# Optimization experiments

Measured on AMD Instinct MI355X. Metric: run time of the kernel, lower is better.

Reference implementation:

```python
import jax, jax.numpy as jnp
import numpy as np

BN_EPS = 1e-5


def _batchnorm(x, gamma, beta):
    # training-mode BatchNorm2d: biased batch stats over (N, H, W)
    mean = jnp.mean(x, axis=(0, 2, 3), keepdims=True)
    var = jnp.var(x, axis=(0, 2, 3), keepdims=True)
    xn = (x - mean) * jax.lax.rsqrt(var + BN_EPS)
    return xn * gamma[None, :, None, None] + beta[None, :, None, None]


def _bin_weight(w):
    # BitConv2d_Robust: w_bin = sign(w) * mean(|w|) per output channel (STE in fwd is just the value)
    alpha = jnp.mean(jnp.abs(w), axis=(1, 2, 3), keepdims=True)
    return jax.lax.stop_gradient(jnp.sign(w) * alpha - w) + w


def _conv(x, w, b, pad):
    y = jax.lax.conv_general_dilated(
        x, w, window_strides=(1, 1), padding=[(pad, pad), (pad, pad)],
        dimension_numbers=('NCHW', 'OIHW', 'NCHW'))
    return y + b[None, :, None, None]


def setup_inputs() -> dict:
    key = jax.random.key(0)
    ks = jax.random.split(key, 14)
    B, Cin, Cout, T, H, W = 16, 128, 256, 512, 64, 64
    fan1 = Cin * 9
    fan2 = Cout * 9
    return {
        'x': jax.random.normal(ks[0], (B, Cin, H, W), jnp.float32),
        't': jax.random.normal(ks[1], (B, T), jnp.float32),
        'bn1_g': jnp.ones((Cin,), jnp.float32),
        'bn1_b': jnp.zeros((Cin,), jnp.float32),
        'w1': jax.random.normal(ks[2], (Cout, Cin, 3, 3), jnp.float32) / np.sqrt(fan1),
        'b1': jax.random.normal(ks[3], (Cout,), jnp.float32) * 0.01,
        'tW': jax.random.normal(ks[4], (Cout, T), jnp.float32) / np.sqrt(T),
        'tb': jax.random.normal(ks[5], (Cout,), jnp.float32) * 0.01,
        'bn2_g': jnp.ones((Cout,), jnp.float32),
        'bn2_b': jnp.zeros((Cout,), jnp.float32),
        'w2': jax.random.normal(ks[6], (Cout, Cout, 3, 3), jnp.float32) / np.sqrt(fan2),
        'b2': jax.random.normal(ks[7], (Cout,), jnp.float32) * 0.01,
        'ws': jax.random.normal(ks[8], (Cout, Cin, 1, 1), jnp.float32) / np.sqrt(Cin),
        'bs': jax.random.normal(ks[9], (Cout,), jnp.float32) * 0.01,
    }


def reference(x, t, bn1_g, bn1_b, w1, b1, tW, tb, bn2_g, bn2_b, w2, b2, ws, bs):
    h = jnp.sign(_batchnorm(x, bn1_g, bn1_b))                # BN + sign binarize
    h = _conv(h, _bin_weight(w1), b1, pad=1)                  # binarized 3x3 conv
    temb = t @ tW.T + tb                                      # time MLP -> [B, Cout]
    h = h + temb[:, :, None, None]
    h = jnp.sign(_batchnorm(h, bn2_g, bn2_b))
    h = _conv(h, _bin_weight(w2), b2, pad=1)
    skip = _conv(x, _bin_weight(ws), bs, pad=0)               # 1x1 binarized skip (in_ch != out_ch)
    return h + skip
```

## Files before the change

kernel.cpp:

```cpp
#include <hip/hip_runtime.h>
#include <stdint.h>

typedef unsigned int uint;
typedef short bf16x8 __attribute__((ext_vector_type(8)));
typedef float f32x4 __attribute__((ext_vector_type(4)));

#define EPS 1e-5f


__global__ __launch_bounds__(256) void k_bn1_part(const float* __restrict__ x, float* __restrict__ part) {
  int c = blockIdx.x, chunk = blockIdx.y;
  float s = 0.f, s2 = 0.f;
  #pragma unroll
  for (int jb = 0; jb < 2; ++jb) {
    int b = chunk * 2 + jb;
    const float4* xb = (const float4*)(x + (((size_t)((b << 7) | c)) << 12));
    #pragma unroll
    for (int k = 0; k < 4; ++k) {
      float4 q = xb[k * 256 + threadIdx.x];
      s += (q.x + q.y) + (q.z + q.w);
      s2 += q.x * q.x + q.y * q.y + q.z * q.z + q.w * q.w;
    }
  }
  #pragma unroll
  for (int off = 32; off > 0; off >>= 1) { s += __shfl_down(s, off); s2 += __shfl_down(s2, off); }
  __shared__ float ls[4], ls2[4];
  int wid = threadIdx.x >> 6, lane = threadIdx.x & 63;
  if (lane == 0) { ls[wid] = s; ls2[wid] = s2; }
  __syncthreads();
  if (threadIdx.x == 0) {
    part[(c * 8 + chunk) * 2 + 0] = ls[0] + ls[1] + ls[2] + ls[3];
    part[(c * 8 + chunk) * 2 + 1] = ls2[0] + ls2[1] + ls2[2] + ls2[3];
  }
}

__global__ void k_bn1_fin(const float* __restrict__ part, const float* __restrict__ g,
                          const float* __restrict__ be, float* __restrict__ sc, float* __restrict__ sh) {
  int c = threadIdx.x;
  float s = 0.f, s2 = 0.f;
  for (int k = 0; k < 8; ++k) { s += part[(c * 8 + k) * 2]; s2 += part[(c * 8 + k) * 2 + 1]; }
  const float inv = 1.f / 65536.f;
  float m = s * inv, var = s2 * inv - m * m;
  float rs = rsqrtf(var + EPS);
  float scale = rs * g[c];
  sc[c] = scale;
  sh[c] = be[c] - m * scale;
}

__global__ __launch_bounds__(128) void k_packw1(const float* __restrict__ w1, uint* __restrict__ wb,
                                                float* __restrict__ alpha, ushort* __restrict__ wT1) {
  int co = blockIdx.x, wid = threadIdx.x >> 6, lane = threadIdx.x & 63;
  int ci = threadIdx.x;
  const float* wp = w1 + (co * 128 + ci) * 9;
  float wv[9]; float s = 0.f;
  #pragma unroll
  for (int tp = 0; tp < 9; ++tp) { wv[tp] = wp[tp]; s += fabsf(wv[tp]); }
  #pragma unroll
  for (int tp = 0; tp < 9; ++tp) {
    wT1[(((tp << 2) + (ci >> 5)) << 13) + (co << 5) + (ci & 31)] = (wv[tp] > 0.f) ? 0x3F80u : 0xBF80u;
    unsigned long long m = __ballot(wv[tp] > 0.f);
    if (lane == 0) {
      wb[(co * 9 + tp) * 4 + wid * 2 + 0] = (uint)m;
      wb[(co * 9 + tp) * 4 + wid * 2 + 1] = (uint)(m >> 32);
    }
  }
  #pragma unroll
  for (int off = 32; off > 0; off >>= 1) s += __shfl_down(s, off);
  __shared__ float l2[2];
  if (lane == 0) l2[wid] = s;
  __syncthreads();
  if (threadIdx.x == 0) alpha[co] = (l2[0] + l2[1]) * (1.f / 1152.f);
}

__global__ __launch_bounds__(256) void k_packw2(const float* __restrict__ w2, uint* __restrict__ wb,
                                                float* __restrict__ alpha, ushort* __restrict__ wT) {
  int co = blockIdx.x, wid = threadIdx.x >> 6, lane = threadIdx.x & 63;
  int ci = threadIdx.x;
  const float* wp = w2 + (co * 256 + ci) * 9;
  float wv[9]; float s = 0.f;
  #pragma unroll
  for (int tp = 0; tp < 9; ++tp) { wv[tp] = wp[tp]; s += fabsf(wv[tp]); }
  int chunk = ci >> 7, kc = (ci >> 5) & 3, cil = ci & 31;
  #pragma unroll
  for (int tp = 0; tp < 9; ++tp) {
    wT[(((tp << 3) + (chunk << 2) + kc) << 13) + (co << 5) + cil] = (wv[tp] > 0.f) ? 0x3F80u : 0xBF80u;
    unsigned long long m = __ballot(wv[tp] > 0.f);
    if (lane == 0) {
      wb[(co * 9 + tp) * 8 + wid * 2 + 0] = (uint)m;
      wb[(co * 9 + tp) * 8 + wid * 2 + 1] = (uint)(m >> 32);
    }
  }
  #pragma unroll
  for (int off = 32; off > 0; off >>= 1) s += __shfl_down(s, off);
  __shared__ float l4[4];
  if (lane == 0) l4[wid] = s;
  __syncthreads();
  if (threadIdx.x == 0) alpha[co] = (l4[0] + l4[1] + l4[2] + l4[3]) * (1.f / 2304.f);
}

__global__ __launch_bounds__(256) void k_base(const uint* __restrict__ wb1, const uint* __restrict__ wb2,
                                              int* __restrict__ base1, int* __restrict__ base2) {
  int co = threadIdx.x;
  int pc1[9], pc2[9];
  #pragma unroll
  for (int tp = 0; tp < 9; ++tp) {
    uint a = 0;
    #pragma unroll
    for (int k = 0; k < 4; ++k) a += __popc(wb1[co * 36 + tp * 4 + k]);
    pc1[tp] = (int)a;
    uint b = 0;
    #pragma unroll
    for (int k = 0; k < 8; ++k) b += __popc(wb2[co * 72 + tp * 8 + k]);
    pc2[tp] = (int)b;
  }
  #pragma unroll
  for (int pat = 0; pat < 9; ++pat) {
    int yt = pat / 3, xt = pat % 3;
    int b1v = 1152, b2v = 2304;
    #pragma unroll
    for (int tp = 0; tp < 9; ++tp) {
      int dy = tp / 3 - 1, dx = tp % 3 - 1;
      bool inv = (dy < 0 && yt == 0) || (dy > 0 && yt == 2) || (dx < 0 && xt == 0) || (dx > 0 && xt == 2);
      if (inv) { b1v -= 128 - 2 * pc1[tp]; b2v -= 256 - 2 * pc2[tp]; }
    }
    base1[pat * 256 + co] = b1v;
    base2[pat * 256 + co] = b2v;
  }
}

__global__ __launch_bounds__(128) void k_packws(const float* __restrict__ wsk, float* __restrict__ swT) {
  int co = blockIdx.x, ci = threadIdx.x;
  float v = wsk[co * 128 + ci];
  float s = fabsf(v);
  #pragma unroll
  for (int off = 32; off > 0; off >>= 1) s += __shfl_down(s, off);
  __shared__ float l2[2]; __shared__ float tot;
  int wid = threadIdx.x >> 6, lane = threadIdx.x & 63;
  if (lane == 0) l2[wid] = s;
  __syncthreads();
  if (threadIdx.x == 0) tot = (l2[0] + l2[1]) * (1.f / 128.f);
  __syncthreads();
  float a = tot;
  swT[ci * 256 + co] = (v > 0.f) ? a : -a;
}

__global__ __launch_bounds__(256) void k_temb(const float* __restrict__ t, const float* __restrict__ tW,
                                              const float* __restrict__ tbias, float* __restrict__ temb) {
  int b = blockIdx.x, co = threadIdx.x;
  const float* tr = t + b * 512;
  const float* wr = tW + co * 512;
  float a0 = 0, a1 = 0, a2 = 0, a3 = 0;
  #pragma unroll 8
  for (int k = 0; k < 512; k += 4) {
    a0 = fmaf(tr[k + 0], wr[k + 0], a0);
    a1 = fmaf(tr[k + 1], wr[k + 1], a1);
    a2 = fmaf(tr[k + 2], wr[k + 2], a2);
    a3 = fmaf(tr[k + 3], wr[k + 3], a3);
  }
  temb[b * 256 + co] = (a0 + a1) + (a2 + a3) + tbias[co];
}

__global__ __launch_bounds__(256, 2) void k_skip(const float* __restrict__ x, const float* __restrict__ swT,
                                                 const float* __restrict__ bsk, const float* __restrict__ b2,
                                                 const float* __restrict__ sc1, const float* __restrict__ sh1,
                                                 uint* __restrict__ sbinw, ushort* __restrict__ h1w,
                                                 int mfma1, float* __restrict__ out) {
  __shared__ float xs[32 * 136];
  __shared__ float wsl[32 * 128];
  int s = blockIdx.x;
  int b = s >> 5;
  int px0 = (s & 31) << 7;
  int co0 = blockIdx.y << 7;
  int t = threadIdx.x;
  int tx = t & 15, ty = t >> 4;

  float4 acc[8][2];
  #pragma unroll
  for (int i = 0; i < 8; ++i) { acc[i][0] = make_float4(0, 0, 0, 0); acc[i][1] = make_float4(0, 0, 0, 0); }

  #pragma unroll 1
  for (int kc = 0; kc < 4; ++kc) {
    if (kc) __syncthreads();
    #pragma unroll
    for (int k2 = 0; k2 < 4; ++k2) {
      int idx = k2 * 256 + t;
      int ci_l = idx >> 5, pxl = (idx & 31) << 2;
      float4 v = *(const float4*)(x + (((size_t)((b << 7) | (kc * 32 + ci_l))) << 12) + px0 + pxl);
      int g = pxl >> 3;
      *(float4*)&xs[ci_l * 136 + g * 8 + ((g >> 2) << 1) + (pxl & 7)] = v;
    }
    #pragma unroll
    for (int k2 = 0; k2 < 4; ++k2) {
      int idx = k2 * 256 + t;
      int ci_l = idx >> 5, col = (idx & 31) << 2;
      *(float4*)&wsl[ci_l * 128 + col] = *(const float4*)(swT + (size_t)(kc * 32 + ci_l) * 256 + co0 + col);
    }
    __syncthreads();

    if (blockIdx.y == 0 && t < 128) {
      int pxl = t;
      int g = pxl >> 3;
      int xo = g * 8 + ((g >> 2) << 1) + (pxl & 7);
      if (mfma1) {
        ushort hv[32];
        #pragma unroll
        for (int i = 0; i < 32; ++i) {
          int ci = kc * 32 + i;
          float v = xs[i * 136 + xo];
          hv[i] = ((v * sc1[ci] + sh1[ci]) > 0.f) ? (ushort)0x3F80u : (ushort)0xBF80u;
        }
        uint4* dst = (uint4*)(h1w + (((size_t)((b << 12) | (px0 + pxl))) << 7) + (kc << 5));
        const uint4* srcv = (const uint4*)hv;
        dst[0] = srcv[0]; dst[1] = srcv[1]; dst[2] = srcv[2]; dst[3] = srcv[3];
      } else {
        uint accb = 0;
        #pragma unroll
        for (int i = 0; i < 32; ++i) {
          int ci = kc * 32 + i;
          float v = xs[i * 136 + xo];
          accb |= ((v * sc1[ci] + sh1[ci]) > 0.f ? 1u : 0u) << i;
        }
        sbinw[(((size_t)b << 12) | (px0 + pxl)) * 4 + kc] = accb;
      }
    }

    int xbase = tx * 8 + ((tx >> 2) << 1);
    int wbase = ty * 8;
    #pragma unroll 2
    for (int ci = 0; ci < 32; ++ci) {
      float4 xv0 = *(float4*)&xs[ci * 136 + xbase];
      float4 xv1 = *(float4*)&xs[ci * 136 + xbase + 4];
      float4 wv0 = *(float4*)&wsl[ci * 128 + wbase];
      float4 wv1 = *(float4*)&wsl[ci * 128 + wbase + 4];
      float wq[8] = {wv0.x, wv0.y, wv0.z, wv0.w, wv1.x, wv1.y, wv1.z, wv1.w};
      #pragma unroll
      for (int i = 0; i < 8; ++i) {
        acc[i][0].x = fmaf(wq[i], xv0.x, acc[i][0].x);
        acc[i][0].y = fmaf(wq[i], xv0.y, acc[i][0].y);
        acc[i][0].z = fmaf(wq[i], xv0.z, acc[i][0].z);
        acc[i][0].w = fmaf(wq[i], xv0.w, acc[i][0].w);
        acc[i][1].x = fmaf(wq[i], xv1.x, acc[i][1].x);
        acc[i][1].y = fmaf(wq[i], xv1.y, acc[i][1].y);
        acc[i][1].z = fmaf(wq[i], xv1.z, acc[i][1].z);
        acc[i][1].w = fmaf(wq[i], xv1.w, acc[i][1].w);
      }
    }
  }

  float* ob = out + ((size_t)b << 20) + px0 + tx * 8;
  #pragma unroll
  for (int i = 0; i < 8; ++i) {
    int co = co0 + ty * 8 + i;
    float bb = bsk[co] + b2[co];
    float4 r0 = acc[i][0]; r0.x += bb; r0.y += bb; r0.z += bb; r0.w += bb;
    float4 r1 = acc[i][1]; r1.x += bb; r1.y += bb; r1.z += bb; r1.w += bb;
    *(float4*)(ob + ((size_t)co << 12)) = r0;
    *(float4*)(ob + ((size_t)co << 12) + 4) = r1;
  }
}

__global__ __launch_bounds__(256, 2) void k_conv1_mfma(const ushort* __restrict__ h1,
                                                       const ushort* __restrict__ wT1,
                                                       short* __restrict__ S1,
                                                       float* __restrict__ part_s,
                                                       float* __restrict__ part_s2) {
  __shared__ ushort act[4 * 66 * 128];
  int bidx = blockIdx.x;
  int s = (bidx & 7) * 64 + (bidx >> 3);
  int b = s >> 5, y0 = (s & 31) << 1;
  int lane = threadIdx.x & 63, wave = threadIdx.x >> 6;
  int co0 = wave << 6;
  int l15 = lane & 15, lk = lane >> 4;

  f32x4 acc[4][8] = {};
  const uint4* h1g = (const uint4*)h1;
  uint4* a4 = (uint4*)act;
  const size_t abase = (size_t)((co0 + l15) << 5) + (lk << 3);

#define LOADAV(dst, ptr)                                                     \
  {                                                                          \
    _Pragma("unroll")                                                        \
    for (int ct_ = 0; ct_ < 4; ++ct_)                                        \
      dst[ct_] = *(const bf16x8*)((ptr) + abase + (ct_ << 9));               \
  }
#define KC_BLOCK(AV, kcv)                                                    \
  {                                                                          \
    _Pragma("unroll")                                                        \
    for (int r_ = 0; r_ < 2; ++r_) {                                         \
      bf16x8 Bv[4];                                                          \
      _Pragma("unroll")                                                      \
      for (int pt_ = 0; pt_ < 4; ++pt_) {                                    \
        int xi_ = (r_ + ty) * 66 + tx + pt_ * 16 + l15;                      \
        int u_ = (((xi_ << 4) + ((kcv) << 2) + lk) ^ (xi_ & 7));             \
        Bv[pt_] = *(bf16x8*)&act[u_ << 3];                                   \
      }                                                                      \
      _Pragma("unroll")                                                      \
      for (int ct_ = 0; ct_ < 4; ++ct_)                                      \
        _Pragma("unroll")                                                    \
        for (int pt_ = 0; pt_ < 4; ++pt_)                                    \
          acc[ct_][r_ * 4 + pt_] = __builtin_amdgcn_mfma_f32_16x16x32_bf16(  \
              AV[ct_], Bv[pt_], acc[ct_][r_ * 4 + pt_], 0, 0, 0);            \
    }                                                                        \
  }

  #pragma unroll 1
  for (int i = 0; i < 17; ++i) {
    int idx = i * 256 + threadIdx.x;
    if (idx < 4224) {
      int q = idx & 15, rowxz = idx >> 4;
      int xz = rowxz % 66, r = rowxz / 66;
      int yy = y0 + r - 1, xx = xz - 1;
      uint4 v = make_uint4(0, 0, 0, 0);
      if (((unsigned)yy < 64u) && ((unsigned)xx < 64u))
        v = h1g[(size_t)((b << 12) | (yy << 6) | xx) * 16 + q];
      a4[((rowxz << 4) + q) ^ (rowxz & 7)] = v;
    }
  }
  __syncthreads();

  bf16x8 AvA[4], AvB[4];
  LOADAV(AvA, wT1);
  #pragma unroll 1
  for (int tp = 0; tp < 9; ++tp) {
    int ty = tp / 3, tx = tp % 3;
    const ushort* wtp = wT1 + ((size_t)tp << 15);
    const ushort* wnx = (tp < 8) ? (wtp + (1 << 15)) : wtp;

    LOADAV(AvB, wtp + (1 << 13));  KC_BLOCK(AvA, 0);
    LOADAV(AvA, wtp + (2 << 13));  KC_BLOCK(AvB, 1);
    LOADAV(AvB, wtp + (3 << 13));  KC_BLOCK(AvA, 2);
    LOADAV(AvA, wnx);              KC_BLOCK(AvB, 3);
  }
#undef LOADAV
#undef KC_BLOCK

  #pragma unroll
  for (int ct = 0; ct < 4; ++ct)
    #pragma unroll
    for (int r = 0; r < 2; ++r)
      #pragma unroll
      for (int pt = 0; pt < 4; ++pt) {
        int x = pt * 16 + l15;
        short* ob = S1 + ((size_t)b << 20) + ((y0 + r) << 6) + x;
        #pragma unroll
        for (int j = 0; j < 4; ++j) {
          int co = co0 + ct * 16 + lk * 4 + j;
          ob[(size_t)co << 12] = (short)acc[ct][r * 4 + pt][j];
        }
      }
  #pragma unroll
  for (int ct = 0; ct < 4; ++ct) {
    float s1v[4] = {0, 0, 0, 0}, s2v[4] = {0, 0, 0, 0};
    #pragma unroll
    for (int k = 0; k < 8; ++k)
      #pragma unroll
      for (int j = 0; j < 4; ++j) {
        float v = acc[ct][k][j];
        s1v[j] += v; s2v[j] += v * v;
      }
    #pragma unroll
    for (int off = 1; off < 16; off <<= 1)
      #pragma unroll
      for (int j = 0; j < 4; ++j) {
        s1v[j] += __shfl_xor(s1v[j], off);
        s2v[j] += __shfl_xor(s2v[j], off);
      }
    if (l15 == 0) {
      #pragma unroll
      for (int j = 0; j < 4; ++j) {
        int co = co0 + ct * 16 + lk * 4 + j;
        part_s[(size_t)s * 256 + co] = s1v[j];
        part_s2[(size_t)s * 256 + co] = s2v[j];
      }
    }
  }
}

__global__ void k_bn2_fin2(const float* __restrict__ part_s, const float* __restrict__ part_s2,
                           const float* __restrict__ al1, const float* __restrict__ b1,
                           const float* __restrict__ g2, const float* __restrict__ be2,
                           const float* __restrict__ temb,
                           float* __restrict__ A, float* __restrict__ Bc, float* __restrict__ Cc) {
  int co = blockIdx.x;
  int t = threadIdx.x;
  float sS = 0.f, scS = 0.f, s2 = 0.f;
  for (int k = 0; k < 8; ++k) {
    int blk = t + k * 64;
    int b = blk >> 5;
    float c = b1[co] + temb[(b << 8) + co];
    float Sv = part_s[(size_t)blk * 256 + co];
    sS += Sv; scS += c * Sv; s2 += part_s2[(size_t)blk * 256 + co];
  }
  #pragma unroll
  for (int off = 32; off > 0; off >>= 1) {
    sS += __shfl_down(sS, off); scS += __shfl_down(scS, off); s2 += __shfl_down(s2, off);
  }
  if (t == 0) {
    float a = al1[co];
    float sumc = 0.f, sumc2 = 0.f;
    for (int b = 0; b < 16; ++b) { float c = b1[co] + temb[(b << 8) + co]; sumc += c; sumc2 += c * c; }
    float sumY = a * sS + 4096.f * sumc;
    float sumY2 = a * a * s2 + 2.f * a * scS + 4096.f * sumc2;
    const float inv = 1.f / 65536.f;
    float m = sumY * inv, var = sumY2 * inv - m * m;
    float rs = rsqrtf(var + EPS);
    float gg = rs * g2[co];
    A[co] = a * gg;
    Bc[co] = (b1[co] - m) * gg + be2[co];
    Cc[co] = gg;
  }
}

__global__ __launch_bounds__(256, 1) void k_conv1(const uint4* __restrict__ sbin, const uint* __restrict__ wb1,
                                                  const int* __restrict__ base1, short* __restrict__ S1) {
  __shared__ uint wlds[32 * 36];
  __shared__ int blds[9 * 32];
  int co0 = blockIdx.y << 5;
  #pragma unroll
  for (int k = 0; k < 4; ++k) wlds[k * 256 + threadIdx.x] = wb1[co0 * 36 + k * 256 + threadIdx.x];
  if (threadIdx.x < 128) wlds[1024 + threadIdx.x] = wb1[co0 * 36 + 1024 + threadIdx.x];
  #pragma unroll
  for (int k = 0; k < 2; ++k) {
    int idx = k * 256 + threadIdx.x;
    if (idx < 288) blds[idx] = base1[(idx >> 5) * 256 + co0 + (idx & 31)];
  }
  int bt = blockIdx.x;
  int b = bt >> 4;
  int y = ((bt & 15) << 2) | (threadIdx.x >> 6);
  int cx = threadIdx.x & 63;
  uint nb[9][4];
  #pragma unroll
  for (int dy = -1; dy <= 1; ++dy)
    #pragma unroll
    for (int dx = -1; dx <= 1; ++dx) {
      int tp = (dy + 1) * 3 + (dx + 1);
      int yy = y + dy, xx = cx + dx;
      bool v = ((unsigned)yy < 64u) && ((unsigned)xx < 64u);
      uint4 q = make_uint4(0, 0, 0, 0);
      if (v) q = sbin[(b << 12) | (yy << 6) | xx];
      nb[tp][0] = q.x; nb[tp][1] = q.y; nb[tp][2] = q.z; nb[tp][3] = q.w;
    }
  int pat = ((y == 0) ? 0 : ((y == 63) ? 6 : 3)) + ((cx == 0) ? 0 : ((cx == 63) ? 2 : 1));
  __syncthreads();
  int p = (y << 6) | cx;
  short* op = S1 + ((size_t)b << 20) + ((size_t)co0 << 12) + p;
  #pragma unroll 1
  for (int cc = 0; cc < 4; ++cc) {
    short accv[8];
    #pragma unroll
    for (int j = 0; j < 8; ++j) {
      int co_l = cc * 8 + j;
      const uint4* wp4 = (const uint4*)(wlds + co_l * 36);
      uint m0 = 0, m1 = 0, m2 = 0, m3 = 0;
      #pragma unroll
      for (int tp = 0; tp < 9; ++tp) {
        uint4 w4 = wp4[tp];
        m0 += __popc(nb[tp][0] ^ w4.x);
        m1 += __popc(nb[tp][1] ^ w4.y);
        m2 += __popc(nb[tp][2] ^ w4.z);
        m3 += __popc(nb[tp][3] ^ w4.w);
      }
      accv[j] = (short)(blds[pat * 32 + co_l] - 2 * (int)((m0 + m1) + (m2 + m3)));
    }
    #pragma unroll
    for (int j = 0; j < 8; ++j) op[(size_t)(cc * 8 + j) << 12] = accv[j];
  }
}

__global__ __launch_bounds__(256) void k_bn2_part(const short* __restrict__ S1, const float* __restrict__ al1,
                                                  const float* __restrict__ b1, const float* __restrict__ temb,
                                                  float* __restrict__ part) {
  int co = blockIdx.x, chunk = blockIdx.y;
  float a = al1[co], bb = b1[co];
  float s = 0.f, s2 = 0.f;
  #pragma unroll
  for (int jb = 0; jb < 2; ++jb) {
    int b = chunk * 2 + jb;
    float tb_ = bb + temb[(b << 8) | co];
    const uint4* sp = (const uint4*)(S1 + ((size_t)b << 20) + ((size_t)co << 12));
    #pragma unroll
    for (int k = 0; k < 2; ++k) {
      uint4 q = sp[k * 256 + threadIdx.x];
      uint ws[4] = {q.x, q.y, q.z, q.w};
      #pragma unroll
      for (int w = 0; w < 4; ++w) {
        float f0 = fmaf(a, (float)((short)(ws[w] & 0xffffu)), tb_);
        float f1 = fmaf(a, (float)((short)(ws[w] >> 16)), tb_);
        s += f0 + f1;
        s2 += f0 * f0 + f1 * f1;
      }
    }
  }
  #pragma unroll
  for (int off = 32; off > 0; off >>= 1) { s += __shfl_down(s, off); s2 += __shfl_down(s2, off); }
  __shared__ float ls[4], ls2[4];
  int wid = threadIdx.x >> 6, lane = threadIdx.x & 63;
  if (lane == 0) { ls[wid] = s; ls2[wid] = s2; }
  __syncthreads();
  if (threadIdx.x == 0) {
    part[(co * 8 + chunk) * 2 + 0] = ls[0] + ls[1] + ls[2] + ls[3];
    part[(co * 8 + chunk) * 2 + 1] = ls2[0] + ls2[1] + ls2[2] + ls2[3];
  }
}

__global__ void k_bn2_fin(const float* __restrict__ part, const float* __restrict__ al1,
                          const float* __restrict__ b1, const float* __restrict__ g2,
                          const float* __restrict__ be2, float* __restrict__ A,
                          float* __restrict__ Bc, float* __restrict__ Cc) {
  int co = threadIdx.x;
  float s = 0.f, s2 = 0.f;
  for (int k = 0; k < 8; ++k) { s += part[(co * 8 + k) * 2]; s2 += part[(co * 8 + k) * 2 + 1]; }
  const float inv = 1.f / 65536.f;
  float m = s * inv, var = s2 * inv - m * m;
  float rs = rsqrtf(var + EPS);
  float gg = rs * g2[co];
  A[co] = al1[co] * gg;
  Bc[co] = (b1[co] - m) * gg + be2[co];
  Cc[co] = gg;
}

__global__ __launch_bounds__(256) void k_bin2_bf16(const short* __restrict__ S1, const float* __restrict__ A,
                                                   const float* __restrict__ Bc, const float* __restrict__ Cc,
                                                   const float* __restrict__ temb, uint4* __restrict__ h2u4) {
  __shared__ uint4 tile[64 * 32];
  int b = blockIdx.x >> 6;
  int px0 = (blockIdx.x & 63) << 6;
  int pxl = threadIdx.x & 63, quad = threadIdx.x >> 6;
  const short* sp = S1 + ((size_t)b << 20) + (px0 + pxl);
  const float* tp = temb + (b << 8);
  #pragma unroll 1
  for (int g = 0; g < 8; ++g) {
    uint d[4];
    #pragma unroll
    for (int h = 0; h < 4; ++h) {
      int c0 = quad * 64 + g * 8 + h * 2;
      float v0 = A[c0] * (float)sp[(size_t)c0 << 12] + Bc[c0] + Cc[c0] * tp[c0];
      float v1 = A[c0 + 1] * (float)sp[(size_t)(c0 + 1) << 12] + Bc[c0 + 1] + Cc[c0 + 1] * tp[c0 + 1];
      uint s0 = (v0 > 0.f) ? 0x3F80u : 0xBF80u;
      uint s1 = (v1 > 0.f) ? 0x3F80u : 0xBF80u;
      d[h] = s0 | (s1 << 16);
    }
    int slot = quad * 8 + g;
    tile[pxl * 32 + (slot ^ (pxl & 7))] = make_uint4(d[0], d[1], d[2], d[3]);
  }
  __syncthreads();
  uint4* dst = h2u4 + ((size_t)(b << 12) + px0) * 32;
  #pragma unroll
  for (int k = 0; k < 8; ++k) {
    int c = k * 256 + threadIdx.x;
    int px = c >> 5, slot = c & 31;
    dst[c] = tile[px * 32 + (slot ^ (px & 7))];
  }
}

__global__ __launch_bounds__(256, 2) void k_conv2_mfma(const ushort* __restrict__ h2,
                                                       const ushort* __restrict__ wT,
                                                       const float* __restrict__ al2,
                                                       float* __restrict__ out) {
  __shared__ ushort act[4 * 66 * 128];
  int bidx = blockIdx.x;
  int s = (bidx & 7) * 64 + (bidx >> 3);
  int b = s >> 5, y0 = (s & 31) << 1;
  int lane = threadIdx.x & 63, wave = threadIdx.x >> 6;
  int co0 = wave << 6;
  int l15 = lane & 15, lk = lane >> 4;

  f32x4 acc[4][8] = {};
  const uint4* h2g = (const uint4*)h2;
  uint4* a4 = (uint4*)act;
  const size_t abase = (size_t)((co0 + l15) << 5) + (lk << 3);

#define LOADAV(dst, ptr)                                                     \
  {                                                                          \
    _Pragma("unroll")                                                        \
    for (int ct_ = 0; ct_ < 4; ++ct_)                                        \
      dst[ct_] = *(const bf16x8*)((ptr) + abase + (ct_ << 9));               \
  }
#define KC_BLOCK(AV, kcv)                                                    \
  {                                                                          \
    _Pragma("unroll")                                                        \
    for (int r_ = 0; r_ < 2; ++r_) {                                         \
      bf16x8 Bv[4];                                                          \
      _Pragma("unroll")                                                      \
      for (int pt_ = 0; pt_ < 4; ++pt_) {                                    \
        int xi_ = (r_ + ty) * 66 + tx + pt_ * 16 + l15;                      \
        int u_ = (((xi_ << 4) + ((kcv) << 2) + lk) ^ (xi_ & 7));             \
        Bv[pt_] = *(bf16x8*)&act[u_ << 3];                                   \
      }                                                                      \
      _Pragma("unroll")                                                      \
      for (int ct_ = 0; ct_ < 4; ++ct_)                                      \
        _Pragma("unroll")                                                    \
        for (int pt_ = 0; pt_ < 4; ++pt_)                                    \
          acc[ct_][r_ * 4 + pt_] = __builtin_amdgcn_mfma_f32_16x16x32_bf16(  \
              AV[ct_], Bv[pt_], acc[ct_][r_ * 4 + pt_], 0, 0, 0);            \
    }                                                                        \
  }

  #pragma unroll 1
  for (int chunk = 0; chunk < 2; ++chunk) {
    if (chunk) __syncthreads();
    #pragma unroll 1
    for (int i = 0; i < 17; ++i) {
      int idx = i * 256 + threadIdx.x;
      if (idx < 4224) {
        int q = idx & 15, rowxz = idx >> 4;
        int xz = rowxz % 66, r = rowxz / 66;
        int yy = y0 + r - 1, xx = xz - 1;
        uint4 v = make_uint4(0, 0, 0, 0);
        if (((unsigned)yy < 64u) && ((unsigned)xx < 64u))
          v = h2g[(size_t)((b << 12) | (yy << 6) | xx) * 32 + chunk * 16 + q];
        a4[((rowxz << 4) + q) ^ (rowxz & 7)] = v;
      }
    }
    __syncthreads();

    const ushort* wch = wT + ((size_t)chunk << 15);
    bf16x8 AvA[4], AvB[4];
    LOADAV(AvA, wch);

    #pragma unroll 1
    for (int tp = 0; tp < 9; ++tp) {
      int ty = tp / 3, tx = tp % 3;
      const ushort* wtp = wch + ((size_t)tp << 16);
      const ushort* wnx = (tp < 8) ? (wtp + (1 << 16)) : wtp;

      LOADAV(AvB, wtp + (1 << 13));  KC_BLOCK(AvA, 0);
      LOADAV(AvA, wtp + (2 << 13));  KC_BLOCK(AvB, 1);
      LOADAV(AvB, wtp + (3 << 13));  KC_BLOCK(AvA, 2);
      LOADAV(AvA, wnx);              KC_BLOCK(AvB, 3);
    }
  }
#undef LOADAV
#undef KC_BLOCK

  #pragma unroll
  for (int ct = 0; ct < 4; ++ct) {
    #pragma unroll
    for (int r = 0; r < 2; ++r) {
      #pragma unroll
      for (int pt = 0; pt < 4; ++pt) {
        int x = pt * 16 + l15;
        float* ob = out + ((size_t)b << 20) + ((y0 + r) << 6) + x;
        #pragma unroll
        for (int j = 0; j < 4; ++j) {
          int co = co0 + ct * 16 + lk * 4 + j;
          float* p = ob + ((size_t)co << 12);
          *p = fmaf(al2[co], acc[ct][r * 4 + pt][j], *p);
        }
      }
    }
  }
}

__global__ __launch_bounds__(256) void k_bin2_packed(const short* __restrict__ S1, const float* __restrict__ A,
                                                     const float* __restrict__ Bc, const float* __restrict__ Cc,
                                                     const float* __restrict__ temb, uint4* __restrict__ hbin) {
  int pg = blockIdx.x * 256 + threadIdx.x;
  int b = pg >> 12, p = pg & 4095;
  int c0 = blockIdx.y << 7;
  const short* sp = S1 + ((size_t)b << 20) + p;
  const float* tp = temb + (b << 8);
  uint w[4];
  #pragma unroll
  for (int wd = 0; wd < 4; ++wd) {
    uint acc = 0;
    #pragma unroll
    for (int i = 0; i < 32; ++i) {
      int co = c0 + wd * 32 + i;
      float v = A[co] * (float)sp[(size_t)co << 12] + Bc[co] + Cc[co] * tp[co];
      acc |= (v > 0.f ? 1u : 0u) << i;
    }
    w[wd] = acc;
  }
  hbin[pg * 2 + blockIdx.y] = make_uint4(w[0], w[1], w[2], w[3]);
}

__global__ __launch_bounds__(256, 1) void k_conv2_pop(const uint4* __restrict__ hbin, const uint* __restrict__ wb2,
                                                      const int* __restrict__ base2, const float* __restrict__ al2,
                                                      float* __restrict__ out) {
  __shared__ uint wlds[32 * 72];
  __shared__ int blds[9 * 32];
  int co0 = blockIdx.y << 5;
  #pragma unroll
  for (int k = 0; k < 9; ++k) wlds[k * 256 + threadIdx.x] = wb2[co0 * 72 + k * 256 + threadIdx.x];
  #pragma unroll
  for (int k = 0; k < 2; ++k) {
    int idx = k * 256 + threadIdx.x;
    if (idx < 288) blds[idx] = base2[(idx >> 5) * 256 + co0 + (idx & 31)];
  }
  int bt = blockIdx.x;
  int b = bt >> 4;
  int y = ((bt & 15) << 2) | (threadIdx.x >> 6);
  int cx = threadIdx.x & 63;
  uint nb[9][8];
  #pragma unroll
  for (int dy = -1; dy <= 1; ++dy)
    #pragma unroll
    for (int dx = -1; dx <= 1; ++dx) {
      int tp = (dy + 1) * 3 + (dx + 1);
      int yy = y + dy, xx = cx + dx;
      bool v = ((unsigned)yy < 64u) && ((unsigned)xx < 64u);
      uint4 q0 = make_uint4(0, 0, 0, 0), q1 = make_uint4(0, 0, 0, 0);
      if (v) {
        int pix = (b << 12) | (yy << 6) | xx;
        q0 = hbin[pix * 2 + 0];
        q1 = hbin[pix * 2 + 1];
      }
      nb[tp][0] = q0.x; nb[tp][1] = q0.y; nb[tp][2] = q0.z; nb[tp][3] = q0.w;
      nb[tp][4] = q1.x; nb[tp][5] = q1.y; nb[tp][6] = q1.z; nb[tp][7] = q1.w;
    }
  int pat = ((y == 0) ? 0 : ((y == 63) ? 6 : 3)) + ((cx == 0) ? 0 : ((cx == 63) ? 2 : 1));
  __syncthreads();
  int p = (y << 6) | cx;
  float* op = out + ((size_t)b << 20) + ((size_t)co0 << 12) + p;
  #pragma unroll 1
  for (int cc = 0; cc < 4; ++cc) {
    float ov[8];
    #pragma unroll
    for (int j = 0; j < 8; ++j) ov[j] = op[(size_t)(cc * 8 + j) << 12];
    #pragma unroll
    for (int j = 0; j < 8; ++j) {
      int co_l = cc * 8 + j;
      const uint4* wp4 = (const uint4*)(wlds + co_l * 72);
      uint m0 = 0, m1 = 0, m2 = 0, m3 = 0;
      #pragma unroll
      for (int tp = 0; tp < 9; ++tp) {
        uint4 wa = wp4[tp * 2 + 0];
        uint4 wb_ = wp4[tp * 2 + 1];
        m0 += __popc(nb[tp][0] ^ wa.x);
        m1 += __popc(nb[tp][1] ^ wa.y);
        m2 += __popc(nb[tp][2] ^ wa.z);
        m3 += __popc(nb[tp][3] ^ wa.w);
        m0 += __popc(nb[tp][4] ^ wb_.x);
        m1 += __popc(nb[tp][5] ^ wb_.y);
        m2 += __popc(nb[tp][6] ^ wb_.z);
        m3 += __popc(nb[tp][7] ^ wb_.w);
      }
      int acc = blds[pat * 32 + co_l] - 2 * (int)((m0 + m1) + (m2 + m3));
      ov[j] = fmaf(al2[co0 + co_l], (float)acc, ov[j]);
    }
    #pragma unroll
    for (int j = 0; j < 8; ++j) op[(size_t)(cc * 8 + j) << 12] = ov[j];
  }
}

extern "C" void kernel_launch(void* const* d_in, const int* in_sizes, int n_in,
                              void* d_out, int out_size, void* d_ws, size_t ws_size,
                              hipStream_t stream) {
  const float* x    = (const float*)d_in[0];
  const float* t    = (const float*)d_in[1];
  const float* bn1g = (const float*)d_in[2];
  const float* bn1b = (const float*)d_in[3];
  const float* w1   = (const float*)d_in[4];
  const float* b1   = (const float*)d_in[5];
  const float* tW   = (const float*)d_in[6];
  const float* tb   = (const float*)d_in[7];
  const float* bn2g = (const float*)d_in[8];
  const float* bn2b = (const float*)d_in[9];
  const float* w2   = (const float*)d_in[10];
  const float* b2   = (const float*)d_in[11];
  const float* wsk  = (const float*)d_in[12];
  const float* bsk  = (const float*)d_in[13];
  float* out = (float*)d_out;
  char* ws = (char*)d_ws;

  float* bn1part = (float*)(ws + 0);
  float* sc1     = (float*)(ws + 8192);
  float* sh1     = (float*)(ws + 8704);
  uint4* sbin    = (uint4*)(ws + 9216);
  uint*  wb1     = (uint*) (ws + 1057792);
  float* al1     = (float*)(ws + 1094656);
  uint*  wb2     = (uint*) (ws + 1095680);
  float* al2     = (float*)(ws + 1169408);
  float* swkT    = (float*)(ws + 1170432);
  float* temb    = (float*)(ws + 1301504);
  float* bn2part = (float*)(ws + 1317888);
  float* A2      = (float*)(ws + 1334272);
  float* Bc2     = (float*)(ws + 1335296);
  float* Cc2     = (float*)(ws + 1336320);
  int*   base1g  = (int*)  (ws + 1337344);
  int*   base2g  = (int*)  (ws + 1346560);
  uint4*  hbin    = (uint4*)(ws + 1355776);
  float*  part_s  = (float*)(ws + 1355776);
  float*  part_s2 = (float*)(ws + 1880064);
  ushort* wT1     = (ushort*)(ws + 2404352);
  ushort* wT2     = (ushort*)(ws + 3452928);
  short*  S1      = (short*)(ws + 4632576);
  ushort* h2      = (ushort*)(ws + 38187008);
  ushort* h1      = (ushort*)(ws + 71741440);
  const size_t WS_NEED2 = 71741440ULL;
  const size_t WS_NEED1 = 88518656ULL;
  bool mode2 = (ws_size >= WS_NEED2);
  bool mode1 = (ws_size >= WS_NEED1);

  k_bn1_part<<<dim3(128, 8), 256, 0, stream>>>(x, bn1part);
  k_bn1_fin<<<1, 128, 0, stream>>>(bn1part, bn1g, bn1b, sc1, sh1);
  k_packw1<<<256, 128, 0, stream>>>(w1, wb1, al1, wT1);
  k_packw2<<<256, 256, 0, stream>>>(w2, wb2, al2, wT2);
  k_base<<<1, 256, 0, stream>>>(wb1, wb2, base1g, base2g);
  k_packws<<<256, 128, 0, stream>>>(wsk, swkT);
  k_temb<<<16, 256, 0, stream>>>(t, tW, tb, temb);
  k_skip<<<dim3(512, 2), 256, 0, stream>>>(x, swkT, bsk, b2, sc1, sh1, (uint*)sbin, h1,
                                           mode1 ? 1 : 0, out);
  if (mode1) {
    k_conv1_mfma<<<512, 256, 0, stream>>>(h1, wT1, S1, part_s, part_s2);
    k_bn2_fin2<<<256, 64, 0, stream>>>(part_s, part_s2, al1, b1, bn2g, bn2b, temb, A2, Bc2, Cc2);
  } else {
    k_conv1<<<dim3(256, 8), 256, 0, stream>>>(sbin, wb1, base1g, S1);
    k_bn2_part<<<dim3(256, 8), 256, 0, stream>>>(S1, al1, b1, temb, bn2part);
    k_bn2_fin<<<1, 256, 0, stream>>>(bn2part, al1, b1, bn2g, bn2b, A2, Bc2, Cc2);
  }
  if (mode2) {
    k_bin2_bf16<<<1024, 256, 0, stream>>>(S1, A2, Bc2, Cc2, temb, (uint4*)h2);
    k_conv2_mfma<<<512, 256, 0, stream>>>(h2, wT2, al2, out);
  } else {
    k_bin2_packed<<<dim3(256, 2), 256, 0, stream>>>(S1, A2, Bc2, Cc2, temb, hbin);
    k_conv2_pop<<<dim3(256, 8), 256, 0, stream>>>(hbin, wb2, base2g, al2, out);
  }
}
```

Measured before the change: 227.2 us.

## Remap conv MFMA waves to 2x2 channel-by-row tiles with 128 channels each

Both MFMA conv kernels now split the four waves as 2 channel groups by 2 output rows, so each wave covers 128 output channels for one row instead of 64 channels for two rows. This halves the LDS activation reads per MFMA and doubles the per-wave weight loads from global. The double-buffered weight prefetch is dropped in favour of loading all 8 A fragments right before use, which may expose global load latency. Conv1 BN partial sums are now combined across the two row-waves through shared memory before being written out.

Result: slower. 298.6 us (+31.4%).

```diff
diff --git a/kernel.cpp b/kernel.cpp
--- a/kernel.cpp
+++ b/kernel.cpp
@@ -259,49 +259,48 @@
   }
 }
 
+#define LOADAV8(dst, ptr)                                                    \
+  {                                                                          \
+    _Pragma("unroll")                                                        \
+    for (int ct_ = 0; ct_ < 8; ++ct_)                                        \
+      dst[ct_] = *(const bf16x8*)((ptr) + abase + (ct_ << 9));               \
+  }
+#define KC_BLOCK8(AV, kcv)                                                   \
+  {                                                                          \
+    bf16x8 Bv[4];                                                            \
+    _Pragma("unroll")                                                        \
+    for (int pt_ = 0; pt_ < 4; ++pt_) {                                      \
+      int xi_ = (wr + ty) * 66 + tx + pt_ * 16 + l15;                        \
+      int u_ = (((xi_ << 4) + ((kcv) << 2) + lk) ^ (xi_ & 7));               \
+      Bv[pt_] = *(bf16x8*)&act[u_ << 3];                                     \
+    }                                                                        \
+    _Pragma("unroll")                                                        \
+    for (int ct_ = 0; ct_ < 8; ++ct_)                                        \
+      _Pragma("unroll")                                                      \
+      for (int pt_ = 0; pt_ < 4; ++pt_)                                      \
+        acc[ct_][pt_] = __builtin_amdgcn_mfma_f32_16x16x32_bf16(             \
+            AV[ct_], Bv[pt_], acc[ct_][pt_], 0, 0, 0);                       \
+  }
+
 __global__ __launch_bounds__(256, 2) void k_conv1_mfma(const ushort* __restrict__ h1,
                                                        const ushort* __restrict__ wT1,
                                                        short* __restrict__ S1,
                                                        float* __restrict__ part_s,
                                                        float* __restrict__ part_s2) {
   __shared__ ushort act[4 * 66 * 128];
+  __shared__ float rbuf_s[512], rbuf_s2[512];
   int bidx = blockIdx.x;
   int s = (bidx & 7) * 64 + (bidx >> 3);
   int b = s >> 5, y0 = (s & 31) << 1;
   int lane = threadIdx.x & 63, wave = threadIdx.x >> 6;
-  int co0 = wave << 6;
+  int wc = wave & 1, wr = wave >> 1;
+  int co0w = wc << 7;
   int l15 = lane & 15, lk = lane >> 4;
 
-  f32x4 acc[4][8] = {};
+  f32x4 acc[8][4] = {};
   const uint4* h1g = (const uint4*)h1;
   uint4* a4 = (uint4*)act;
-  const size_t abase = (size_t)((co0 + l15) << 5) + (lk << 3);
-
-#define LOADAV(dst, ptr)                                                     \
-  {                                                                          \
-    _Pragma("unroll")                                                        \
-    for (int ct_ = 0; ct_ < 4; ++ct_)                                        \
-      dst[ct_] = *(const bf16x8*)((ptr) + abase + (ct_ << 9));               \
-  }
-#define KC_BLOCK(AV, kcv)                                                    \
-  {                                                                          \
-    _Pragma("unroll")                                                        \
-    for (int r_ = 0; r_ < 2; ++r_) {                                         \
-      bf16x8 Bv[4];                                                          \
-      _Pragma("unroll")                                                      \
-      for (int pt_ = 0; pt_ < 4; ++pt_) {                                    \
-        int xi_ = (r_ + ty) * 66 + tx + pt_ * 16 + l15;                      \
-        int u_ = (((xi_ << 4) + ((kcv) << 2) + lk) ^ (xi_ & 7));             \
-        Bv[pt_] = *(bf16x8*)&act[u_ << 3];                                   \
-      }                                                                      \
-      _Pragma("unroll")                                                      \
-      for (int ct_ = 0; ct_ < 4; ++ct_)                                      \
-        _Pragma("unroll")                                                    \
-        for (int pt_ = 0; pt_ < 4; ++pt_)                                    \
-          acc[ct_][r_ * 4 + pt_] = __builtin_amdgcn_mfma_f32_16x16x32_bf16(  \
-              AV[ct_], Bv[pt_], acc[ct_][r_ * 4 + pt_], 0, 0, 0);            \
-    }                                                                        \
-  }
+  const size_t abase = (size_t)((co0w + l15) << 5) + (lk << 3);
 
   #pragma unroll 1
   for (int i = 0; i < 17; ++i) {
@@ -318,44 +317,37 @@
   }
   __syncthreads();
 
-  bf16x8 AvA[4], AvB[4];
-  LOADAV(AvA, wT1);
+  bf16x8 Av[8];
   #pragma unroll 1
   for (int tp = 0; tp < 9; ++tp) {
     int ty = tp / 3, tx = tp % 3;
     const ushort* wtp = wT1 + ((size_t)tp << 15);
-    const ushort* wnx = (tp < 8) ? (wtp + (1 << 15)) : wtp;
-
-    LOADAV(AvB, wtp + (1 << 13));  KC_BLOCK(AvA, 0);
-    LOADAV(AvA, wtp + (2 << 13));  KC_BLOCK(AvB, 1);
-    LOADAV(AvB, wtp + (3 << 13));  KC_BLOCK(AvA, 2);
-    LOADAV(AvA, wnx);              KC_BLOCK(AvB, 3);
-  }
-#undef LOADAV
-#undef KC_BLOCK
-
-  #pragma unroll
-  for (int ct = 0; ct < 4; ++ct)
-    #pragma unroll
-    for (int r = 0; r < 2; ++r)
-      #pragma unroll
-      for (int pt = 0; pt < 4; ++pt) {
-        int x = pt * 16 + l15;
-        short* ob = S1 + ((size_t)b << 20) + ((y0 + r) << 6) + x;
-        #pragma unroll
-        for (int j = 0; j < 4; ++j) {
-          int co = co0 + ct * 16 + lk * 4 + j;
-          ob[(size_t)co << 12] = (short)acc[ct][r * 4 + pt][j];
-        }
-      }
-  #pragma unroll
-  for (int ct = 0; ct < 4; ++ct) {
+    LOADAV8(Av, wtp);              KC_BLOCK8(Av, 0);
+    LOADAV8(Av, wtp + (1 << 13));  KC_BLOCK8(Av, 1);
+    LOADAV8(Av, wtp + (2 << 13));  KC_BLOCK8(Av, 2);
+    LOADAV8(Av, wtp + (3 << 13));  KC_BLOCK8(Av, 3);
+  }
+
+  short* ob = S1 + ((size_t)b << 20) + ((y0 + wr) << 6);
+  #pragma unroll
+  for (int ct = 0; ct < 8; ++ct)
+    #pragma unroll
+    for (int pt = 0; pt < 4; ++pt) {
+      int x = pt * 16 + l15;
+      #pragma unroll
+      for (int j = 0; j < 4; ++j) {
+        int co = co0w + ct * 16 + lk * 4 + j;
+        ob[((size_t)co << 12) + x] = (short)acc[ct][pt][j];
+      }
+    }
+  #pragma unroll
+  for (int ct = 0; ct < 8; ++ct) {
     float s1v[4] = {0, 0, 0, 0}, s2v[4] = {0, 0, 0, 0};
     #pragma unroll
-    for (int k = 0; k < 8; ++k)
+    for (int pt = 0; pt < 4; ++pt)
       #pragma unroll
       for (int j = 0; j < 4; ++j) {
-        float v = acc[ct][k][j];
+        float v = acc[ct][pt][j];
         s1v[j] += v; s2v[j] += v * v;
       }
     #pragma unroll
@@ -368,11 +360,18 @@
     if (l15 == 0) {
       #pragma unroll
       for (int j = 0; j < 4; ++j) {
-        int co = co0 + ct * 16 + lk * 4 + j;
-        part_s[(size_t)s * 256 + co] = s1v[j];
-        part_s2[(size_t)s * 256 + co] = s2v[j];
-      }
-    }
+        int idx = wave * 128 + ct * 16 + lk * 4 + j;
+        rbuf_s[idx] = s1v[j];
+        rbuf_s2[idx] = s2v[j];
+      }
+    }
+  }
+  __syncthreads();
+  if (threadIdx.x < 256) {
+    int co = threadIdx.x;
+    int wcc = co >> 7, col = co & 127;
+    part_s[(size_t)s * 256 + co] = rbuf_s[wcc * 128 + col] + rbuf_s[(wcc + 2) * 128 + col];
+    part_s2[(size_t)s * 256 + co] = rbuf_s2[wcc * 128 + col] + rbuf_s2[(wcc + 2) * 128 + col];
   }
 }
 
@@ -562,39 +561,14 @@
   int s = (bidx & 7) * 64 + (bidx >> 3);
   int b = s >> 5, y0 = (s & 31) << 1;
   int lane = threadIdx.x & 63, wave = threadIdx.x >> 6;
-  int co0 = wave << 6;
+  int wc = wave & 1, wr = wave >> 1;
+  int co0w = wc << 7;
   int l15 = lane & 15, lk = lane >> 4;
 
-  f32x4 acc[4][8] = {};
+  f32x4 acc[8][4] = {};
   const uint4* h2g = (const uint4*)h2;
   uint4* a4 = (uint4*)act;
-  const size_t abase = (size_t)((co0 + l15) << 5) + (lk << 3);
-
-#define LOADAV(dst, ptr)                                                     \
-  {                                                                          \
-    _Pragma("unroll")                                                        \
-    for (int ct_ = 0; ct_ < 4; ++ct_)                                        \
-      dst[ct_] = *(const bf16x8*)((ptr) + abase + (ct_ << 9));               \
-  }
-#define KC_BLOCK(AV, kcv)                                                    \
-  {                                                                          \
-    _Pragma("unroll")                                                        \
-    for (int r_ = 0; r_ < 2; ++r_) {                                         \
-      bf16x8 Bv[4];                                                          \
-      _Pragma("unroll")                                                      \
-      for (int pt_ = 0; pt_ < 4; ++pt_) {                                    \
-        int xi_ = (r_ + ty) * 66 + tx + pt_ * 16 + l15;                      \
-        int u_ = (((xi_ << 4) + ((kcv) << 2) + lk) ^ (xi_ & 7));             \
-        Bv[pt_] = *(bf16x8*)&act[u_ << 3];                                   \
-      }                                                                      \
-      _Pragma("unroll")                                                      \
-      for (int ct_ = 0; ct_ < 4; ++ct_)                                      \
-        _Pragma("unroll")                                                    \
-        for (int pt_ = 0; pt_ < 4; ++pt_)                                    \
-          acc[ct_][r_ * 4 + pt_] = __builtin_amdgcn_mfma_f32_16x16x32_bf16(  \
-              AV[ct_], Bv[pt_], acc[ct_][r_ * 4 + pt_], 0, 0, 0);            \
-    }                                                                        \
-  }
+  const size_t abase = (size_t)((co0w + l15) << 5) + (lk << 3);
 
   #pragma unroll 1
   for (int chunk = 0; chunk < 2; ++chunk) {
@@ -615,38 +589,29 @@
     __syncthreads();
 
     const ushort* wch = wT + ((size_t)chunk << 15);
-    bf16x8 AvA[4], AvB[4];
-    LOADAV(AvA, wch);
-
+    bf16x8 Av[8];
     #pragma unroll 1
     for (int tp = 0; tp < 9; ++tp) {
       int ty = tp / 3, tx = tp % 3;
       const ushort* wtp = wch + ((size_t)tp << 16);
-      const ushort* wnx = (tp < 8) ? (wtp + (1 << 16)) : wtp;
-
-      LOADAV(AvB, wtp + (1 << 13));  KC_BLOCK(AvA, 0);
-      LOADAV(AvA, wtp + (2 << 13));  KC_BLOCK(AvB, 1);
-      LOADAV(AvB, wtp + (3 << 13));  KC_BLOCK(AvA, 2);
-      LOADAV(AvA, wnx);              KC_BLOCK(AvB, 3);
-    }
-  }
-#undef LOADAV
-#undef KC_BLOCK
-
-  #pragma unroll
-  for (int ct = 0; ct < 4; ++ct) {
-    #pragma unroll
-    for (int r = 0; r < 2; ++r) {
-      #pragma unroll
-      for (int pt = 0; pt < 4; ++pt) {
-        int x = pt * 16 + l15;
-        float* ob = out + ((size_t)b << 20) + ((y0 + r) << 6) + x;
-        #pragma unroll
-        for (int j = 0; j < 4; ++j) {
-          int co = co0 + ct * 16 + lk * 4 + j;
-          float* p = ob + ((size_t)co << 12);
-          *p = fmaf(al2[co], acc[ct][r * 4 + pt][j], *p);
-        }
+      LOADAV8(Av, wtp);              KC_BLOCK8(Av, 0);
+      LOADAV8(Av, wtp + (1 << 13));  KC_BLOCK8(Av, 1);
+      LOADAV8(Av, wtp + (2 << 13));  KC_BLOCK8(Av, 2);
+      LOADAV8(Av, wtp + (3 << 13));  KC_BLOCK8(Av, 3);
+    }
+  }
+
+  float* ob = out + ((size_t)b << 20) + ((y0 + wr) << 6);
+  #pragma unroll
+  for (int ct = 0; ct < 8; ++ct) {
+    #pragma unroll
+    for (int pt = 0; pt < 4; ++pt) {
+      int x = pt * 16 + l15;
+      #pragma unroll
+      for (int j = 0; j < 4; ++j) {
+        int co = co0w + ct * 16 + lk * 4 + j;
+        float* p = ob + ((size_t)co << 12) + x;
+        *p = fmaf(al2[co], acc[ct][pt][j], *p);
       }
     }
   }
```

## Retile conv2 waves as 2x2 over channels and rows

Applied to the files above, without the earlier changes.

Reassigns each wave in the conv2 MFMA kernel to cover 128 output channels for one output row, instead of 64 channels across both rows. This halves the LDS activation fragment reads per wave. It doubles the weight fragment loads from global memory and the registers held for double-buffered weights. The higher register use may strain the two-blocks-per-CU occupancy target.

Result: slower. 271.8 us (+19.6%).

```diff
diff --git a/kernel.cpp b/kernel.cpp
--- a/kernel.cpp
+++ b/kernel.cpp
@@ -553,6 +553,29 @@
   }
 }
 
+#define LOADAV8(dst, ptr)                                                    \
+  {                                                                          \
+    _Pragma("unroll")                                                        \
+    for (int ct_ = 0; ct_ < 8; ++ct_)                                        \
+      dst[ct_] = *(const bf16x8*)((ptr) + abase + (ct_ << 9));               \
+  }
+#define KC_BLOCK8(AV, kcv)                                                   \
+  {                                                                          \
+    bf16x8 Bv[4];                                                            \
+    _Pragma("unroll")                                                        \
+    for (int pt_ = 0; pt_ < 4; ++pt_) {                                      \
+      int xi_ = (wr + ty) * 66 + tx + pt_ * 16 + l15;                        \
+      int u_ = (((xi_ << 4) + ((kcv) << 2) + lk) ^ (xi_ & 7));               \
+      Bv[pt_] = *(bf16x8*)&act[u_ << 3];                                     \
+    }                                                                        \
+    _Pragma("unroll")                                                        \
+    for (int ct_ = 0; ct_ < 8; ++ct_)                                        \
+      _Pragma("unroll")                                                      \
+      for (int pt_ = 0; pt_ < 4; ++pt_)                                      \
+        acc[ct_][pt_] = __builtin_amdgcn_mfma_f32_16x16x32_bf16(             \
+            AV[ct_], Bv[pt_], acc[ct_][pt_], 0, 0, 0);                       \
+  }
+
 __global__ __launch_bounds__(256, 2) void k_conv2_mfma(const ushort* __restrict__ h2,
                                                        const ushort* __restrict__ wT,
                                                        const float* __restrict__ al2,
@@ -562,39 +585,14 @@
   int s = (bidx & 7) * 64 + (bidx >> 3);
   int b = s >> 5, y0 = (s & 31) << 1;
   int lane = threadIdx.x & 63, wave = threadIdx.x >> 6;
-  int co0 = wave << 6;
+  int wc = wave & 1, wr = wave >> 1;
+  int co0w = wc << 7;
   int l15 = lane & 15, lk = lane >> 4;
 
-  f32x4 acc[4][8] = {};
+  f32x4 acc[8][4] = {};
   const uint4* h2g = (const uint4*)h2;
   uint4* a4 = (uint4*)act;
-  const size_t abase = (size_t)((co0 + l15) << 5) + (lk << 3);
-
-#define LOADAV(dst, ptr)                                                     \
-  {                                                                          \
-    _Pragma("unroll")                                                        \
-    for (int ct_ = 0; ct_ < 4; ++ct_)                                        \
-      dst[ct_] = *(const bf16x8*)((ptr) + abase + (ct_ << 9));               \
-  }
-#define KC_BLOCK(AV, kcv)                                                    \
-  {                                                                          \
-    _Pragma("unroll")                                                        \
-    for (int r_ = 0; r_ < 2; ++r_) {                                         \
-      bf16x8 Bv[4];                                                          \
-      _Pragma("unroll")                                                      \
-      for (int pt_ = 0; pt_ < 4; ++pt_) {                                    \
-        int xi_ = (r_ + ty) * 66 + tx + pt_ * 16 + l15;                      \
-        int u_ = (((xi_ << 4) + ((kcv) << 2) + lk) ^ (xi_ & 7));             \
-        Bv[pt_] = *(bf16x8*)&act[u_ << 3];                                   \
-      }                                                                      \
-      _Pragma("unroll")                                                      \
-      for (int ct_ = 0; ct_ < 4; ++ct_)                                      \
-        _Pragma("unroll")                                                    \
-        for (int pt_ = 0; pt_ < 4; ++pt_)                                    \
-          acc[ct_][r_ * 4 + pt_] = __builtin_amdgcn_mfma_f32_16x16x32_bf16(  \
-              AV[ct_], Bv[pt_], acc[ct_][r_ * 4 + pt_], 0, 0, 0);            \
-    }                                                                        \
-  }
+  const size_t abase = (size_t)((co0w + l15) << 5) + (lk << 3);
 
   #pragma unroll 1
   for (int chunk = 0; chunk < 2; ++chunk) {
@@ -615,38 +613,32 @@
     __syncthreads();
 
     const ushort* wch = wT + ((size_t)chunk << 15);
-    bf16x8 AvA[4], AvB[4];
-    LOADAV(AvA, wch);
-
+    bf16x8 AvA[8], AvB[8];
+    LOADAV8(AvA, wch);
     #pragma unroll 1
     for (int tp = 0; tp < 9; ++tp) {
       int ty = tp / 3, tx = tp % 3;
       const ushort* wtp = wch + ((size_t)tp << 16);
       const ushort* wnx = (tp < 8) ? (wtp + (1 << 16)) : wtp;
 
-      LOADAV(AvB, wtp + (1 << 13));  KC_BLOCK(AvA, 0);
-      LOADAV(AvA, wtp + (2 << 13));  KC_BLOCK(AvB, 1);
-      LOADAV(AvB, wtp + (3 << 13));  KC_BLOCK(AvA, 2);
-      LOADAV(AvA, wnx);              KC_BLOCK(AvB, 3);
-    }
-  }
-#undef LOADAV
-#undef KC_BLOCK
-
-  #pragma unroll
-  for (int ct = 0; ct < 4; ++ct) {
-    #pragma unroll
-    for (int r = 0; r < 2; ++r) {
+      LOADAV8(AvB, wtp + (1 << 13));  KC_BLOCK8(AvA, 0);
+      LOADAV8(AvA, wtp + (2 << 13));  KC_BLOCK8(AvB, 1);
+      LOADAV8(AvB, wtp + (3 << 13));  KC_BLOCK8(AvA, 2);
+      LOADAV8(AvA, wnx);              KC_BLOCK8(AvB, 3);
+    }
+  }
+
+  float* ob = out + ((size_t)b << 20) + ((y0 + wr) << 6);
+  #pragma unroll
+  for (int ct = 0; ct < 8; ++ct) {
+    #pragma unroll
+    for (int pt = 0; pt < 4; ++pt) {
+      int x = pt * 16 + l15;
       #pragma unroll
-      for (int pt = 0; pt < 4; ++pt) {
-        int x = pt * 16 + l15;
-        float* ob = out + ((size_t)b << 20) + ((y0 + r) << 6) + x;
-        #pragma unroll
-        for (int j = 0; j < 4; ++j) {
-          int co = co0 + ct * 16 + lk * 4 + j;
-          float* p = ob + ((size_t)co << 12);
-          *p = fmaf(al2[co], acc[ct][r * 4 + pt][j], *p);
-        }
+      for (int j = 0; j < 4; ++j) {
+        int co = co0w + ct * 16 + lk * 4 + j;
+        float* p = ob + ((size_t)co << 12) + x;
+        *p = fmaf(al2[co], acc[ct][pt][j], *p);
       }
     }
   }
```
